# Kernel optimization log

Measured on AMD Instinct MI355X. Metric: run time of the kernel, lower is better.

The kernel has to match this reference:

```python
import jax, jax.numpy as jnp
import numpy as np

N_NODES = 4_000_000
N_GRAPHS = 4096  # B; fixed for jit (torch derives it from batch.max()+1)
D_FEAT = 8
NUM_CLASSES = 10


def setup_inputs() -> dict:
    key = jax.random.key(0)
    k1, k2, k3, k4, k5 = jax.random.split(key, 5)
    x = jax.random.normal(k1, (N_NODES, D_FEAT), dtype=jnp.float32)
    # sorted segment ids; with ~977 nodes/graph expected, empty segments are vanishingly unlikely
    batch_ids = jnp.sort(jax.random.randint(k2, (N_NODES,), 0, N_GRAPHS, dtype=jnp.int64))
    input_ids = jax.random.randint(k3, (N_GRAPHS, 128), 0, 30522, dtype=jnp.int64)
    attention_mask = jnp.ones((N_GRAPHS, 128), dtype=jnp.int64)
    W = jax.random.normal(k4, (NUM_CLASSES, D_FEAT), dtype=jnp.float32) * (1.0 / np.sqrt(D_FEAT))
    b = jax.random.normal(k5, (NUM_CLASSES,), dtype=jnp.float32) * 0.01
    return {"x": x, "batch_ids": batch_ids, "input_ids": input_ids,
            "attention_mask": attention_mask, "W": W, "b": b}


def reference(x, batch_ids, input_ids, attention_mask, W, b):
    # Segment-mean pooling: replaces the O(B) python loop of masked means
    # with a single-pass scatter-add. input_ids / attention_mask are unused
    # by the original forward (kept for signature fidelity).
    sums = jax.ops.segment_sum(x, batch_ids, num_segments=N_GRAPHS)          # [B, 8]
    counts = jax.ops.segment_sum(jnp.ones((x.shape[0],), x.dtype), batch_ids,
                                 num_segments=N_GRAPHS)                      # [B]
    pooled = sums / counts[:, None]                                          # [B, 8]
    logits = pooled @ W.T + b                                                # [B, 10]
    return logits
```

## Files before the change

### kernel.cpp

```cpp
#include <hip/hip_runtime.h>

constexpr int N_NODES  = 4000000;
constexpr int N_GRAPHS = 4096;
constexpr int D_FEAT   = 8;
constexpr int N_CLS    = 10;
constexpr int WIN      = 16384;

typedef float f32x4 __attribute__((ext_vector_type(4)));

__global__ __launch_bounds__(256) void fused_pool_linear(
    const float* __restrict__ x,
    const int*   __restrict__ ids,
    const float* __restrict__ W,
    const float* __restrict__ bias,
    float*       __restrict__ out)
{
    const f32x4* xf = (const f32x4*)x;
    int g    = blockIdx.x;
    int lane = threadIdx.x & 63;
    int half = lane >> 5;
    int l32  = lane & 31;
    int target = g + half;

    int est = (int)((long long)target * N_NODES / N_GRAPHS);
    int lo = est - WIN; if (lo < 0) lo = 0;
    int hi = est + WIN; if (hi > N_NODES) hi = N_NODES;
    {
        bool okL = (lo == 0)       || (ids[lo - 1] < target);
        bool okR = (hi == N_NODES) || (ids[hi] >= target);
        if (!(okL && okR)) { lo = 0; hi = N_NODES; }
    }

    while (hi - lo > 32) {
        int chunk = (hi - lo + 31) >> 5;
        int pos = lo + l32 * chunk;
        int v = (pos < hi) ? ids[pos] : 0x7fffffff;
        unsigned long long m = __ballot(v < target);
        unsigned int mm = half ? (unsigned int)(m >> 32) : (unsigned int)m;
        int cnt = __popc(mm);
        int nlo = cnt ? lo + (cnt - 1) * chunk + 1 : lo;
        int nhi = (cnt < 32) ? min(lo + cnt * chunk, hi) : hi;
        lo = nlo; hi = nhi;
    }
    {
        int pos = lo + l32;
        int v = (pos < hi) ? ids[pos] : 0x7fffffff;
        unsigned long long m = __ballot(v < target);
        unsigned int mm = half ? (unsigned int)(m >> 32) : (unsigned int)m;
        lo += __popc(mm);
    }
    int s = __shfl(lo, 0);
    int e = __shfl(lo, 32);
    int len  = e - s;
    int endf = 2 * e;

    f32x4 a0 = (f32x4)(0.f), a1 = (f32x4)(0.f),
          a2 = (f32x4)(0.f), a3 = (f32x4)(0.f);
    for (int i = 2 * s + (int)threadIdx.x; i < endf; i += 1024) {
        a0 += xf[i];
        if (i + 256 < endf) a1 += xf[i + 256];
        if (i + 512 < endf) a2 += xf[i + 512];
        if (i + 768 < endf) a3 += xf[i + 768];
    }
    f32x4 acc = (a0 + a1) + (a2 + a3);

    #pragma unroll
    for (int off = 32; off >= 2; off >>= 1) {
        acc.x += __shfl_xor(acc.x, off);
        acc.y += __shfl_xor(acc.y, off);
        acc.z += __shfl_xor(acc.z, off);
        acc.w += __shfl_xor(acc.w, off);
    }
    f32x4 other;
    other.x = __shfl_xor(acc.x, 1);
    other.y = __shfl_xor(acc.y, 1);
    other.z = __shfl_xor(acc.z, 1);
    other.w = __shfl_xor(acc.w, 1);

    __shared__ float red[4][D_FEAT];
    __shared__ float mean[D_FEAT];
    int wid = threadIdx.x >> 6;
    if (lane == 0) {
        red[wid][0] = acc.x;   red[wid][1] = acc.y;
        red[wid][2] = acc.z;   red[wid][3] = acc.w;
        red[wid][4] = other.x; red[wid][5] = other.y;
        red[wid][6] = other.z; red[wid][7] = other.w;
    }
    __syncthreads();
    if (threadIdx.x < D_FEAT) {
        float v = red[0][threadIdx.x] + red[1][threadIdx.x]
                + red[2][threadIdx.x] + red[3][threadIdx.x];
        mean[threadIdx.x] = v / (float)len;
    }
    __syncthreads();
    if (threadIdx.x < N_CLS) {
        const float* w = W + (size_t)threadIdx.x * D_FEAT;
        float a = bias[threadIdx.x];
        #pragma unroll
        for (int j = 0; j < D_FEAT; ++j)
            a += mean[j] * w[j];
        out[(size_t)g * N_CLS + threadIdx.x] = a;
    }
}

extern "C" void kernel_launch(void* const* d_in, const int* in_sizes, int n_in,
                              void* d_out, int out_size, void* d_ws, size_t ws_size,
                              hipStream_t stream) {
    const float* x   = (const float*)d_in[0];
    const int*   ids = (const int*)d_in[1];
    const float* W   = (const float*)d_in[4];
    const float* b   = (const float*)d_in[5];
    float*       out = (float*)d_out;

    fused_pool_linear<<<N_GRAPHS, 256, 0, stream>>>(x, ids, W, b, out);
}
```

Measured before the change: 33.66 us.

## Assign one graph per wavefront, four graphs per block

Each 64-lane wavefront now handles one whole graph, doing its own binary search and reduction, so a 256-thread block covers four graphs and the grid shrinks by four. Previously all four wavefronts of a block searched for the same boundaries redundantly and had to be combined through shared memory with an extra barrier. The cost is that each graph's ~1000 rows are now streamed by only 64 lanes, which gives less memory-level parallelism per graph and lets uneven segment sizes unbalance the waves within a block.

```diff
diff --git a/kernel.cpp b/kernel.cpp
--- a/kernel.cpp
+++ b/kernel.cpp
@@ -4,6 +4,7 @@
 constexpr int N_GRAPHS = 4096;
 constexpr int D_FEAT   = 8;
 constexpr int N_CLS    = 10;
+constexpr int GPB      = 4;
 constexpr int WIN      = 16384;
 
 typedef float f32x4 __attribute__((ext_vector_type(4)));
@@ -16,8 +17,10 @@
     float*       __restrict__ out)
 {
     const f32x4* xf = (const f32x4*)x;
-    int g    = blockIdx.x;
+    int wid  = threadIdx.x >> 6;
     int lane = threadIdx.x & 63;
+    int g    = blockIdx.x * GPB + wid;
+
     int half = lane >> 5;
     int l32  = lane & 31;
     int target = g + half;
@@ -56,11 +59,11 @@
 
     f32x4 a0 = (f32x4)(0.f), a1 = (f32x4)(0.f),
           a2 = (f32x4)(0.f), a3 = (f32x4)(0.f);
-    for (int i = 2 * s + (int)threadIdx.x; i < endf; i += 1024) {
+    for (int i = 2 * s + lane; i < endf; i += 256) {
         a0 += xf[i];
-        if (i + 256 < endf) a1 += xf[i + 256];
-        if (i + 512 < endf) a2 += xf[i + 512];
-        if (i + 768 < endf) a3 += xf[i + 768];
+        if (i +  64 < endf) a1 += xf[i +  64];
+        if (i + 128 < endf) a2 += xf[i + 128];
+        if (i + 192 < endf) a3 += xf[i + 192];
     }
     f32x4 acc = (a0 + a1) + (a2 + a3);
 
@@ -77,29 +80,26 @@
     other.z = __shfl_xor(acc.z, 1);
     other.w = __shfl_xor(acc.w, 1);
 
-    __shared__ float red[4][D_FEAT];
-    __shared__ float mean[D_FEAT];
-    int wid = threadIdx.x >> 6;
+    __shared__ float red[GPB][D_FEAT];
+    __shared__ float linv[GPB];
     if (lane == 0) {
         red[wid][0] = acc.x;   red[wid][1] = acc.y;
         red[wid][2] = acc.z;   red[wid][3] = acc.w;
         red[wid][4] = other.x; red[wid][5] = other.y;
         red[wid][6] = other.z; red[wid][7] = other.w;
+        linv[wid]   = 1.0f / (float)len;
     }
     __syncthreads();
-    if (threadIdx.x < D_FEAT) {
-        float v = red[0][threadIdx.x] + red[1][threadIdx.x]
-                + red[2][threadIdx.x] + red[3][threadIdx.x];
-        mean[threadIdx.x] = v / (float)len;
-    }
-    __syncthreads();
-    if (threadIdx.x < N_CLS) {
-        const float* w = W + (size_t)threadIdx.x * D_FEAT;
-        float a = bias[threadIdx.x];
+    if (threadIdx.x < GPB * N_CLS) {
+        int j = threadIdx.x / N_CLS;
+        int c = threadIdx.x % N_CLS;
+        float inv = linv[j];
+        const float* w = W + (size_t)c * D_FEAT;
+        float a = bias[c];
         #pragma unroll
-        for (int j = 0; j < D_FEAT; ++j)
-            a += mean[j] * w[j];
-        out[(size_t)g * N_CLS + threadIdx.x] = a;
+        for (int k = 0; k < D_FEAT; ++k)
+            a += (red[j][k] * inv) * w[k];
+        out[((size_t)blockIdx.x * GPB + j) * N_CLS + c] = a;
     }
 }
 
@@ -112,5 +112,5 @@
     const float* b   = (const float*)d_in[5];
     float*       out = (float*)d_out;
 
-    fused_pool_linear<<<N_GRAPHS, 256, 0, stream>>>(x, ids, W, b, out);
+    fused_pool_linear<<<N_GRAPHS / GPB, 256, 0, stream>>>(x, ids, W, b, out);
 }
```

Result: faster. 29.89 us (-11.2%).
